# Kernel tuning notes

Measured on AMD Instinct MI355X. Metric: run time of the kernel, lower is better.

The kernel has to match this reference:

```python
import jax, jax.numpy as jnp
import numpy as np

FEATURES = 32
RES = 512
TIME_DIM = 16
N_PTS = 1048576


def _sample_plane(plane, gx, gy):
    """Bilinear grid_sample, align_corners=True.
    plane: (C, H, W); gx in [-1,1] indexes W, gy in [-1,1] indexes H.
    Returns (N, C).
    """
    C, H, W = plane.shape
    ix = (gx + 1.0) * 0.5 * (W - 1)
    iy = (gy + 1.0) * 0.5 * (H - 1)
    ix0f = jnp.clip(jnp.floor(ix), 0, W - 1)
    iy0f = jnp.clip(jnp.floor(iy), 0, H - 1)
    ix0 = ix0f.astype(jnp.int32)
    iy0 = iy0f.astype(jnp.int32)
    ix1 = jnp.minimum(ix0 + 1, W - 1)
    iy1 = jnp.minimum(iy0 + 1, H - 1)
    wx = ix - ix0f  # (N,)
    wy = iy - iy0f
    v00 = plane[:, iy0, ix0]  # (C, N)
    v01 = plane[:, iy0, ix1]
    v10 = plane[:, iy1, ix0]
    v11 = plane[:, iy1, ix1]
    out = (v00 * ((1 - wx) * (1 - wy)) + v01 * (wx * (1 - wy))
           + v10 * ((1 - wx) * wy) + v11 * (wx * wy))
    return out.T  # (N, C)


def setup_inputs() -> dict:
    key = jax.random.key(0)
    ks = jax.random.split(key, 7)
    x = jax.random.uniform(ks[0], (N_PTS, 4), dtype=jnp.float32, minval=-1.0, maxval=1.0)
    plane_xy = jax.random.normal(ks[1], (FEATURES, RES, RES), dtype=jnp.float32)
    plane_xz = jax.random.normal(ks[2], (FEATURES, RES, RES), dtype=jnp.float32)
    plane_yz = jax.random.normal(ks[3], (FEATURES, RES, RES), dtype=jnp.float32)
    plane_xt = jax.random.normal(ks[4], (FEATURES, RES, TIME_DIM), dtype=jnp.float32)
    plane_yt = jax.random.normal(ks[5], (FEATURES, RES, TIME_DIM), dtype=jnp.float32)
    plane_zt = jax.random.normal(ks[6], (FEATURES, RES, TIME_DIM), dtype=jnp.float32)
    return {"x": x, "plane_xy": plane_xy, "plane_xz": plane_xz, "plane_yz": plane_yz,
            "plane_xt": plane_xt, "plane_yt": plane_yt, "plane_zt": plane_zt}


def reference(x, plane_xy, plane_xz, plane_yz, plane_xt, plane_yt, plane_zt):
    center, scale = 0.0, 2.0
    u = (x - center) / scale + 0.5   # map to [0,1]
    g = u * 2.0 - 1.0                # back to [-1,1] grid coords
    gx, gy, gz, gt = g[:, 0], g[:, 1], g[:, 2], g[:, 3]
    feat_xy = _sample_plane(plane_xy, gx, gy)
    feat_xz = _sample_plane(plane_xz, gx, gz)
    feat_yz = _sample_plane(plane_yz, gy, gz)
    feat_xt = _sample_plane(plane_xt, gx, gt)
    feat_yt = _sample_plane(plane_yt, gy, gt)
    feat_zt = _sample_plane(plane_zt, gz, gt)
    return jnp.concatenate([feat_xy, feat_xz, feat_yz, feat_xt, feat_yt, feat_zt], axis=1)
```

## Files before the change

kernel.cpp:

```cpp
#include <hip/hip_runtime.h>
#include <stdint.h>

#define NPTS 1048576

using u16x8 = __attribute__((ext_vector_type(8))) unsigned short;
using f32x4 = __attribute__((ext_vector_type(4))) float;

__device__ __forceinline__ float bf2f(unsigned short u) {
    union { unsigned int i; float f; } c; c.i = ((unsigned int)u) << 16; return c.f;
}
__device__ __forceinline__ unsigned int f2bf_bits(float f) {
    union { float f; unsigned int i; } c; c.f = f;
    unsigned int i = c.i;
    i += 0x7fffu + ((i >> 16) & 1u);
    return i >> 16;
}

template<int WC, int H, int W>
__global__ __launch_bounds__(256) void transpose3(const float* __restrict__ s0,
                                                  const float* __restrict__ s1,
                                                  const float* __restrict__ s2,
                                                  unsigned short* __restrict__ dst) {
    __shared__ float tile[32][WC + 1];
    const float* src = (blockIdx.y == 0) ? s0 : (blockIdx.y == 1) ? s1 : s2;
    constexpr int CH = W / WC;
    const int h  = blockIdx.x / CH;
    const int w0 = (blockIdx.x % CH) * WC;
    const int HW = H * W;
    const float* s = src + h * W + w0;
    for (int i = threadIdx.x; i < 32 * WC; i += 256) {
        int c = i / WC, w = i - c * WC;
        tile[c][w] = s[c * HW + w];
    }
    __syncthreads();
    unsigned int* d = (unsigned int*)(dst + (size_t)blockIdx.y * HW * 32
                                          + (size_t)(h * W + w0) * 32);
    for (int i = threadIdx.x; i < 16 * WC; i += 256) {
        int w = i >> 4, cp = i & 15;
        unsigned int lo = f2bf_bits(tile[cp * 2][w]);
        unsigned int hi = f2bf_bits(tile[cp * 2 + 1][w]);
        d[i] = lo | (hi << 16);
    }
}

template<int W, int H>
__device__ __forceinline__ void sample_one(const unsigned short* __restrict__ pl,
                                           float gw, float gh, int sub,
                                           float* __restrict__ o) {
    float ix = (gw + 1.0f) * 0.5f * (float)(W - 1);
    float iy = (gh + 1.0f) * 0.5f * (float)(H - 1);
    float fx0 = fminf(fmaxf(floorf(ix), 0.0f), (float)(W - 1));
    float fy0 = fminf(fmaxf(floorf(iy), 0.0f), (float)(H - 1));
    int ix0 = (int)fx0, iy0 = (int)fy0;
    int ix1 = min(ix0 + 1, W - 1), iy1 = min(iy0 + 1, H - 1);
    float wx = ix - fx0, wy = iy - fy0;
    float wx0 = 1.0f - wx, wy0 = 1.0f - wy;
    float w00 = wx0 * wy0, w01 = wx * wy0, w10 = wx0 * wy, w11 = wx * wy;
    const int base = sub * 8;
    u16x8 v00 = *(const u16x8*)(pl + ((iy0 * W + ix0) * 32 + base));
    u16x8 v01 = *(const u16x8*)(pl + ((iy0 * W + ix1) * 32 + base));
    u16x8 v10 = *(const u16x8*)(pl + ((iy1 * W + ix0) * 32 + base));
    u16x8 v11 = *(const u16x8*)(pl + ((iy1 * W + ix1) * 32 + base));
    f32x4 r0, r1;
#pragma unroll
    for (int j = 0; j < 4; ++j)
        r0[j] = bf2f(v00[j]) * w00 + bf2f(v01[j]) * w01
              + bf2f(v10[j]) * w10 + bf2f(v11[j]) * w11;
#pragma unroll
    for (int j = 0; j < 4; ++j)
        r1[j] = bf2f(v00[4 + j]) * w00 + bf2f(v01[4 + j]) * w01
              + bf2f(v10[4 + j]) * w10 + bf2f(v11[4 + j]) * w11;
    *(f32x4*)(o)     = r0;
    *(f32x4*)(o + 4) = r1;
}

__global__ __launch_bounds__(256) void sample_kernel(const float* __restrict__ x,
                                                     const unsigned short* __restrict__ ws,
                                                     float* __restrict__ out) {
    int tid = blockIdx.x * 256 + threadIdx.x;
    int p   = tid >> 2;
    int sub = tid & 3;
    f32x4 xv = *(const f32x4*)(x + (size_t)p * 4);
    float gx = (xv[0] * 0.5f + 0.5f) * 2.0f - 1.0f;
    float gy = (xv[1] * 0.5f + 0.5f) * 2.0f - 1.0f;
    float gz = (xv[2] * 0.5f + 0.5f) * 2.0f - 1.0f;
    float gt = (xv[3] * 0.5f + 0.5f) * 2.0f - 1.0f;
    float* o = out + (size_t)p * 192 + sub * 8;
    sample_one<512, 512>(ws + 0ul,        gx, gy, sub, o + 0);
    sample_one<512, 512>(ws + 8388608ul,  gx, gz, sub, o + 32);
    sample_one<512, 512>(ws + 16777216ul, gy, gz, sub, o + 64);
    sample_one<16,  512>(ws + 25165824ul, gx, gt, sub, o + 96);
    sample_one<16,  512>(ws + 25427968ul, gy, gt, sub, o + 128);
    sample_one<16,  512>(ws + 25690112ul, gz, gt, sub, o + 160);
}

template<int W, int H>
__device__ __forceinline__ void sample_direct_one(const float* __restrict__ pl,
                                                  float gw, float gh, int sub,
                                                  float* __restrict__ o) {
    float ix = (gw + 1.0f) * 0.5f * (float)(W - 1);
    float iy = (gh + 1.0f) * 0.5f * (float)(H - 1);
    float fx0 = fminf(fmaxf(floorf(ix), 0.0f), (float)(W - 1));
    float fy0 = fminf(fmaxf(floorf(iy), 0.0f), (float)(H - 1));
    int ix0 = (int)fx0, iy0 = (int)fy0;
    int ix1 = min(ix0 + 1, W - 1), iy1 = min(iy0 + 1, H - 1);
    float wx = ix - fx0, wy = iy - fy0;
    float wx0 = 1.0f - wx, wy0 = 1.0f - wy;
    float w00 = wx0 * wy0, w01 = wx * wy0, w10 = wx0 * wy, w11 = wx * wy;
    const int HW = W * H;
    int a00 = iy0 * W + ix0, a01 = iy0 * W + ix1;
    int a10 = iy1 * W + ix0, a11 = iy1 * W + ix1;
    const float* b = pl + (size_t)sub * 8 * HW;
#pragma unroll
    for (int j = 0; j < 8; ++j) {
        o[j] = b[a00] * w00 + b[a01] * w01 + b[a10] * w10 + b[a11] * w11;
        b += HW;
    }
}

__global__ __launch_bounds__(256) void sample_fallback(const float* __restrict__ x,
    const float* __restrict__ pxy, const float* __restrict__ pxz,
    const float* __restrict__ pyz, const float* __restrict__ pxt,
    const float* __restrict__ pyt, const float* __restrict__ pzt,
    float* __restrict__ out) {
    int tid = blockIdx.x * 256 + threadIdx.x;
    int p   = tid >> 2;
    int sub = tid & 3;
    f32x4 xv = *(const f32x4*)(x + (size_t)p * 4);
    float gx = (xv[0] * 0.5f + 0.5f) * 2.0f - 1.0f;
    float gy = (xv[1] * 0.5f + 0.5f) * 2.0f - 1.0f;
    float gz = (xv[2] * 0.5f + 0.5f) * 2.0f - 1.0f;
    float gt = (xv[3] * 0.5f + 0.5f) * 2.0f - 1.0f;
    float* o = out + (size_t)p * 192 + sub * 8;
    sample_direct_one<512, 512>(pxy, gx, gy, sub, o + 0);
    sample_direct_one<512, 512>(pxz, gx, gz, sub, o + 32);
    sample_direct_one<512, 512>(pyz, gy, gz, sub, o + 64);
    sample_direct_one<16,  512>(pxt, gx, gt, sub, o + 96);
    sample_direct_one<16,  512>(pyt, gy, gt, sub, o + 128);
    sample_direct_one<16,  512>(pzt, gz, gt, sub, o + 160);
}

extern "C" void kernel_launch(void* const* d_in, const int* in_sizes, int n_in,
                              void* d_out, int out_size, void* d_ws, size_t ws_size,
                              hipStream_t stream) {
    const float* x   = (const float*)d_in[0];
    const float* pxy = (const float*)d_in[1];
    const float* pxz = (const float*)d_in[2];
    const float* pyz = (const float*)d_in[3];
    const float* pxt = (const float*)d_in[4];
    const float* pyt = (const float*)d_in[5];
    const float* pzt = (const float*)d_in[6];
    float* out = (float*)d_out;

    const size_t need_elems = 25952256ull;
    const size_t need_bytes = need_elems * 2;

    if (ws_size >= need_bytes) {
        unsigned short* ws = (unsigned short*)d_ws;
        transpose3<64, 512, 512><<<dim3(512 * 8, 3), 256, 0, stream>>>(pxy, pxz, pyz, ws);
        transpose3<16, 512, 16><<<dim3(512, 3), 256, 0, stream>>>(pxt, pyt, pzt, ws + 25165824ul);
        sample_kernel<<<(NPTS * 4) / 256, 256, 0, stream>>>(x, ws, out);
    } else {
        sample_fallback<<<(NPTS * 4) / 256, 256, 0, stream>>>(x, pxy, pxz, pyz, pxt, pyt, pzt, out);
    }
}
```

Measured before the change: 394.0 us.

## Sort points by Morton bin before sampling to improve gather locality

Adds a counting sort of query points into 32^3 Morton-ordered spatial bins (histogram, single-block scan, atomic scatter), then samples in sorted order and writes each result back to its original row. Neighbouring threads then gather nearby plane texels, which is meant to raise cache hit rates for the random bilinear gathers over roughly 50 MB of bf16 planes. Output stores become nontemporal, and workgroups are swizzled across XCDs. The cost is three extra kernels, a memset, atomics, and scattered output writes, and the larger workspace must be available for the new path to run.

```diff
diff --git a/kernel.cpp b/kernel.cpp
--- a/kernel.cpp
+++ b/kernel.cpp
@@ -2,9 +2,18 @@
 #include <stdint.h>
 
 #define NPTS 1048576
+#define NBINS 32768
 
 using u16x8 = __attribute__((ext_vector_type(8))) unsigned short;
 using f32x4 = __attribute__((ext_vector_type(4))) float;
+
+#define OFF_HIST     51904512ul
+#define OFF_CURSOR   52035584ul
+#define OFF_KEYS     52166656ul
+#define OFF_XS       54263808ul
+#define OFF_PID      71041024ul
+#define WS_NEED_FULL 75235328ul
+#define WS_NEED_MID  51904512ul
 
 __device__ __forceinline__ float bf2f(unsigned short u) {
     union { unsigned int i; float f; } c; c.i = ((unsigned int)u) << 16; return c.f;
@@ -14,6 +23,13 @@
     unsigned int i = c.i;
     i += 0x7fffu + ((i >> 16) & 1u);
     return i >> 16;
+}
+__device__ __forceinline__ unsigned int spread3(unsigned int v) {
+    v &= 31u;
+    v = (v | (v << 8)) & 0x100Fu;
+    v = (v | (v << 4)) & 0x10C3u;
+    v = (v | (v << 2)) & 0x1249u;
+    return v;
 }
 
 template<int WC, int H, int W>
@@ -43,7 +59,56 @@
     }
 }
 
-template<int W, int H>
+__global__ __launch_bounds__(256) void hist_kernel(const float* __restrict__ x,
+                                                   unsigned int* __restrict__ hist,
+                                                   unsigned short* __restrict__ keys) {
+    int p = blockIdx.x * 256 + threadIdx.x;
+    f32x4 xv = *(const f32x4*)(x + (size_t)p * 4);
+    int bx = min(31, max(0, (int)((xv[0] + 1.0f) * 16.0f)));
+    int by = min(31, max(0, (int)((xv[1] + 1.0f) * 16.0f)));
+    int bz = min(31, max(0, (int)((xv[2] + 1.0f) * 16.0f)));
+    unsigned int key = (spread3(bx) << 2) | (spread3(by) << 1) | spread3(bz);
+    keys[p] = (unsigned short)key;
+    atomicAdd(&hist[key], 1u);
+}
+
+__global__ __launch_bounds__(1024) void scan_kernel(const unsigned int* __restrict__ hist,
+                                                    unsigned int* __restrict__ cursor) {
+    __shared__ unsigned int part[1024];
+    int t = threadIdx.x;
+    unsigned int local[32];
+    unsigned int s = 0;
+    int base = t * 32;
+#pragma unroll
+    for (int j = 0; j < 32; ++j) { local[j] = s; s += hist[base + j]; }
+    part[t] = s;
+    __syncthreads();
+    for (int off = 1; off < 1024; off <<= 1) {
+        unsigned int v = 0;
+        if (t >= off) v = part[t - off];
+        __syncthreads();
+        if (t >= off) part[t] += v;
+        __syncthreads();
+    }
+    unsigned int chunkbase = part[t] - s;
+#pragma unroll
+    for (int j = 0; j < 32; ++j) cursor[base + j] = chunkbase + local[j];
+}
+
+__global__ __launch_bounds__(256) void scatter_kernel(const float* __restrict__ x,
+                                                      const unsigned short* __restrict__ keys,
+                                                      unsigned int* __restrict__ cursor,
+                                                      f32x4* __restrict__ xs,
+                                                      unsigned int* __restrict__ pid) {
+    int p = blockIdx.x * 256 + threadIdx.x;
+    f32x4 xv = *(const f32x4*)(x + (size_t)p * 4);
+    unsigned int k = keys[p];
+    unsigned int pos = atomicAdd(&cursor[k], 1u);
+    xs[pos] = xv;
+    pid[pos] = (unsigned int)p;
+}
+
+template<int W, int H, bool NT>
 __device__ __forceinline__ void sample_one(const unsigned short* __restrict__ pl,
                                            float gw, float gh, int sub,
                                            float* __restrict__ o) {
@@ -70,8 +135,44 @@
     for (int j = 0; j < 4; ++j)
         r1[j] = bf2f(v00[4 + j]) * w00 + bf2f(v01[4 + j]) * w01
               + bf2f(v10[4 + j]) * w10 + bf2f(v11[4 + j]) * w11;
-    *(f32x4*)(o)     = r0;
-    *(f32x4*)(o + 4) = r1;
+    if (NT) {
+        __builtin_nontemporal_store(r0, (f32x4*)(o));
+        __builtin_nontemporal_store(r1, (f32x4*)(o + 4));
+    } else {
+        *(f32x4*)(o)     = r0;
+        *(f32x4*)(o + 4) = r1;
+    }
+}
+
+__device__ __forceinline__ void sample_all(f32x4 xv, int sub,
+                                           const unsigned short* __restrict__ ws,
+                                           float* __restrict__ o) {
+    float gx = (xv[0] * 0.5f + 0.5f) * 2.0f - 1.0f;
+    float gy = (xv[1] * 0.5f + 0.5f) * 2.0f - 1.0f;
+    float gz = (xv[2] * 0.5f + 0.5f) * 2.0f - 1.0f;
+    float gt = (xv[3] * 0.5f + 0.5f) * 2.0f - 1.0f;
+    sample_one<512, 512, true>(ws + 0ul,        gx, gy, sub, o + 0);
+    sample_one<512, 512, true>(ws + 8388608ul,  gx, gz, sub, o + 32);
+    sample_one<512, 512, true>(ws + 16777216ul, gy, gz, sub, o + 64);
+    sample_one<16,  512, true>(ws + 25165824ul, gx, gt, sub, o + 96);
+    sample_one<16,  512, true>(ws + 25427968ul, gy, gt, sub, o + 128);
+    sample_one<16,  512, true>(ws + 25690112ul, gz, gt, sub, o + 160);
+}
+
+__global__ __launch_bounds__(256) void sample_sorted(const f32x4* __restrict__ xs,
+                                                     const unsigned int* __restrict__ pid,
+                                                     const unsigned short* __restrict__ ws,
+                                                     float* __restrict__ out) {
+    int nwg = gridDim.x;
+    int cpx = nwg >> 3;
+    int bid = blockIdx.x;
+    int swz = (bid & 7) * cpx + (bid >> 3);
+    int tid = swz * 256 + threadIdx.x;
+    int s   = tid >> 2;
+    int sub = tid & 3;
+    f32x4 xv = xs[s];
+    int p = pid[s];
+    sample_all(xv, sub, ws, out + (size_t)p * 192 + sub * 8);
 }
 
 __global__ __launch_bounds__(256) void sample_kernel(const float* __restrict__ x,
@@ -81,17 +182,7 @@
     int p   = tid >> 2;
     int sub = tid & 3;
     f32x4 xv = *(const f32x4*)(x + (size_t)p * 4);
-    float gx = (xv[0] * 0.5f + 0.5f) * 2.0f - 1.0f;
-    float gy = (xv[1] * 0.5f + 0.5f) * 2.0f - 1.0f;
-    float gz = (xv[2] * 0.5f + 0.5f) * 2.0f - 1.0f;
-    float gt = (xv[3] * 0.5f + 0.5f) * 2.0f - 1.0f;
-    float* o = out + (size_t)p * 192 + sub * 8;
-    sample_one<512, 512>(ws + 0ul,        gx, gy, sub, o + 0);
-    sample_one<512, 512>(ws + 8388608ul,  gx, gz, sub, o + 32);
-    sample_one<512, 512>(ws + 16777216ul, gy, gz, sub, o + 64);
-    sample_one<16,  512>(ws + 25165824ul, gx, gt, sub, o + 96);
-    sample_one<16,  512>(ws + 25427968ul, gy, gt, sub, o + 128);
-    sample_one<16,  512>(ws + 25690112ul, gz, gt, sub, o + 160);
+    sample_all(xv, sub, ws, out + (size_t)p * 192 + sub * 8);
 }
 
 template<int W, int H>
@@ -152,14 +243,27 @@
     const float* pzt = (const float*)d_in[6];
     float* out = (float*)d_out;
 
-    const size_t need_elems = 25952256ull;
-    const size_t need_bytes = need_elems * 2;
-
-    if (ws_size >= need_bytes) {
-        unsigned short* ws = (unsigned short*)d_ws;
-        transpose3<64, 512, 512><<<dim3(512 * 8, 3), 256, 0, stream>>>(pxy, pxz, pyz, ws);
-        transpose3<16, 512, 16><<<dim3(512, 3), 256, 0, stream>>>(pxt, pyt, pzt, ws + 25165824ul);
-        sample_kernel<<<(NPTS * 4) / 256, 256, 0, stream>>>(x, ws, out);
+    if (ws_size >= WS_NEED_FULL) {
+        char* wsb = (char*)d_ws;
+        unsigned short* planes = (unsigned short*)wsb;
+        unsigned int*   hist   = (unsigned int*)(wsb + OFF_HIST);
+        unsigned int*   cursor = (unsigned int*)(wsb + OFF_CURSOR);
+        unsigned short* keys   = (unsigned short*)(wsb + OFF_KEYS);
+        f32x4*          xs     = (f32x4*)(wsb + OFF_XS);
+        unsigned int*   pid    = (unsigned int*)(wsb + OFF_PID);
+
+        hipMemsetAsync(hist, 0, NBINS * sizeof(unsigned int), stream);
+        transpose3<64, 512, 512><<<dim3(512 * 8, 3), 256, 0, stream>>>(pxy, pxz, pyz, planes);
+        transpose3<16, 512, 16><<<dim3(512, 3), 256, 0, stream>>>(pxt, pyt, pzt, planes + 25165824ul);
+        hist_kernel<<<NPTS / 256, 256, 0, stream>>>(x, hist, keys);
+        scan_kernel<<<1, 1024, 0, stream>>>(hist, cursor);
+        scatter_kernel<<<NPTS / 256, 256, 0, stream>>>(x, keys, cursor, xs, pid);
+        sample_sorted<<<(NPTS * 4) / 256, 256, 0, stream>>>(xs, pid, planes, out);
+    } else if (ws_size >= WS_NEED_MID) {
+        unsigned short* planes = (unsigned short*)d_ws;
+        transpose3<64, 512, 512><<<dim3(512 * 8, 3), 256, 0, stream>>>(pxy, pxz, pyz, planes);
+        transpose3<16, 512, 16><<<dim3(512, 3), 256, 0, stream>>>(pxt, pyt, pzt, planes + 25165824ul);
+        sample_kernel<<<(NPTS * 4) / 256, 256, 0, stream>>>(x, planes, out);
     } else {
         sample_fallback<<<(NPTS * 4) / 256, 256, 0, stream>>>(x, pxy, pxz, pyz, pxt, pyt, pzt, out);
     }
```

Result: faster. 372.6 us (-5.4%).

## Store horizontally duplicated texel pairs in bf16 workspace to halve gather addresses

Applied to the files above, without the earlier changes.

Adds a transpose pass that writes each texel together with its right neighbour, 64 bf16 channels per entry. Each corner pair (x0,x1) then comes from one contiguous 128-byte span, so the sampler needs two distinct row addresses instead of four scattered ones, which should cut cache-line fetches for the random gathers. In exchange the workspace doubles to about 104 MB and the transpose writes twice as many bytes. Output stores also become nontemporal.

```diff
diff --git a/kernel.cpp b/kernel.cpp
--- a/kernel.cpp
+++ b/kernel.cpp
@@ -5,6 +5,22 @@
 
 using u16x8 = __attribute__((ext_vector_type(8))) unsigned short;
 using f32x4 = __attribute__((ext_vector_type(4))) float;
+
+#define DUP_XY 0ul
+#define DUP_XZ 16777216ul
+#define DUP_YZ 33554432ul
+#define DUP_XT 50331648ul
+#define DUP_YT 50855936ul
+#define DUP_ZT 51380224ul
+#define WS_NEED_FULL 103809024ul
+
+#define PL_XY 0ul
+#define PL_XZ 8388608ul
+#define PL_YZ 16777216ul
+#define PL_XT 25165824ul
+#define PL_YT 25427968ul
+#define PL_ZT 25690112ul
+#define WS_NEED_MID  51904512ul
 
 __device__ __forceinline__ float bf2f(unsigned short u) {
     union { unsigned int i; float f; } c; c.i = ((unsigned int)u) << 16; return c.f;
@@ -14,6 +30,88 @@
     unsigned int i = c.i;
     i += 0x7fffu + ((i >> 16) & 1u);
     return i >> 16;
+}
+
+template<int WC, int W>
+__global__ __launch_bounds__(256) void transpose_dup(const float* __restrict__ s0,
+                                                     const float* __restrict__ s1,
+                                                     const float* __restrict__ s2,
+                                                     unsigned short* __restrict__ dst,
+                                                     size_t planeStride) {
+    __shared__ float tile[32][WC + 2];
+    const float* src = (blockIdx.y == 0) ? s0 : (blockIdx.y == 1) ? s1 : s2;
+    constexpr int CH = W / WC;
+    const int h  = blockIdx.x / CH;
+    const int w0 = (blockIdx.x % CH) * WC;
+    const int HW = 512 * W;
+    for (int i = threadIdx.x; i < 32 * (WC + 1); i += 256) {
+        int c = i / (WC + 1), w = i - c * (WC + 1);
+        int gw = min(w0 + w, W - 1);
+        tile[c][w] = src[c * HW + h * W + gw];
+    }
+    __syncthreads();
+    unsigned int* d = (unsigned int*)(dst + blockIdx.y * planeStride
+                                          + (size_t)(h * W + w0) * 64);
+    for (int idx = threadIdx.x; idx < WC * 32; idx += 256) {
+        int blk = idx >> 5, j = idx & 31;
+        int texsel = j >> 4, chp = j & 15;
+        int col = blk + texsel;
+        unsigned int lo = f2bf_bits(tile[chp * 2][col]);
+        unsigned int hi = f2bf_bits(tile[chp * 2 + 1][col]);
+        d[idx] = lo | (hi << 16);
+    }
+}
+
+template<int W>
+__device__ __forceinline__ void sample_dup(const unsigned short* __restrict__ pl,
+                                           float gw, float gh, int sub,
+                                           float* __restrict__ o) {
+    float ix = (gw + 1.0f) * 0.5f * (float)(W - 1);
+    float iy = (gh + 1.0f) * 0.5f * 511.0f;
+    float fx0 = fminf(fmaxf(floorf(ix), 0.0f), (float)(W - 1));
+    float fy0 = fminf(fmaxf(floorf(iy), 0.0f), 511.0f);
+    int ix0 = (int)fx0, iy0 = (int)fy0;
+    int iy1 = min(iy0 + 1, 511);
+    float wx = ix - fx0, wy = iy - fy0;
+    float wx0 = 1.0f - wx, wy0 = 1.0f - wy;
+    float w00 = wx0 * wy0, w01 = wx * wy0, w10 = wx0 * wy, w11 = wx * wy;
+    const unsigned short* b0 = pl + ((size_t)(iy0 * W + ix0) << 6) + sub * 8;
+    const unsigned short* b1 = pl + ((size_t)(iy1 * W + ix0) << 6) + sub * 8;
+    u16x8 v00 = *(const u16x8*)(b0);
+    u16x8 v01 = *(const u16x8*)(b0 + 32);
+    u16x8 v10 = *(const u16x8*)(b1);
+    u16x8 v11 = *(const u16x8*)(b1 + 32);
+    f32x4 r0, r1;
+#pragma unroll
+    for (int j = 0; j < 4; ++j)
+        r0[j] = bf2f(v00[j]) * w00 + bf2f(v01[j]) * w01
+              + bf2f(v10[j]) * w10 + bf2f(v11[j]) * w11;
+#pragma unroll
+    for (int j = 0; j < 4; ++j)
+        r1[j] = bf2f(v00[4 + j]) * w00 + bf2f(v01[4 + j]) * w01
+              + bf2f(v10[4 + j]) * w10 + bf2f(v11[4 + j]) * w11;
+    __builtin_nontemporal_store(r0, (f32x4*)(o));
+    __builtin_nontemporal_store(r1, (f32x4*)(o + 4));
+}
+
+__global__ __launch_bounds__(256) void sample_dup_kernel(const float* __restrict__ x,
+                                                         const unsigned short* __restrict__ ws,
+                                                         float* __restrict__ out) {
+    int tid = blockIdx.x * 256 + threadIdx.x;
+    int p   = tid >> 2;
+    int sub = tid & 3;
+    f32x4 xv = *(const f32x4*)(x + (size_t)p * 4);
+    float gx = (xv[0] * 0.5f + 0.5f) * 2.0f - 1.0f;
+    float gy = (xv[1] * 0.5f + 0.5f) * 2.0f - 1.0f;
+    float gz = (xv[2] * 0.5f + 0.5f) * 2.0f - 1.0f;
+    float gt = (xv[3] * 0.5f + 0.5f) * 2.0f - 1.0f;
+    float* o = out + (size_t)p * 192 + sub * 8;
+    sample_dup<512>(ws + DUP_XY, gx, gy, sub, o + 0);
+    sample_dup<512>(ws + DUP_XZ, gx, gz, sub, o + 32);
+    sample_dup<512>(ws + DUP_YZ, gy, gz, sub, o + 64);
+    sample_dup<16 >(ws + DUP_XT, gx, gt, sub, o + 96);
+    sample_dup<16 >(ws + DUP_YT, gy, gt, sub, o + 128);
+    sample_dup<16 >(ws + DUP_ZT, gz, gt, sub, o + 160);
 }
 
 template<int WC, int H, int W>
@@ -86,12 +184,12 @@
     float gz = (xv[2] * 0.5f + 0.5f) * 2.0f - 1.0f;
     float gt = (xv[3] * 0.5f + 0.5f) * 2.0f - 1.0f;
     float* o = out + (size_t)p * 192 + sub * 8;
-    sample_one<512, 512>(ws + 0ul,        gx, gy, sub, o + 0);
-    sample_one<512, 512>(ws + 8388608ul,  gx, gz, sub, o + 32);
-    sample_one<512, 512>(ws + 16777216ul, gy, gz, sub, o + 64);
-    sample_one<16,  512>(ws + 25165824ul, gx, gt, sub, o + 96);
-    sample_one<16,  512>(ws + 25427968ul, gy, gt, sub, o + 128);
-    sample_one<16,  512>(ws + 25690112ul, gz, gt, sub, o + 160);
+    sample_one<512, 512>(ws + PL_XY, gx, gy, sub, o + 0);
+    sample_one<512, 512>(ws + PL_XZ, gx, gz, sub, o + 32);
+    sample_one<512, 512>(ws + PL_YZ, gy, gz, sub, o + 64);
+    sample_one<16,  512>(ws + PL_XT, gx, gt, sub, o + 96);
+    sample_one<16,  512>(ws + PL_YT, gy, gt, sub, o + 128);
+    sample_one<16,  512>(ws + PL_ZT, gz, gt, sub, o + 160);
 }
 
 template<int W, int H>
@@ -152,14 +250,18 @@
     const float* pzt = (const float*)d_in[6];
     float* out = (float*)d_out;
 
-    const size_t need_elems = 25952256ull;
-    const size_t need_bytes = need_elems * 2;
-
-    if (ws_size >= need_bytes) {
+    if (ws_size >= WS_NEED_FULL) {
         unsigned short* ws = (unsigned short*)d_ws;
-        transpose3<64, 512, 512><<<dim3(512 * 8, 3), 256, 0, stream>>>(pxy, pxz, pyz, ws);
-        transpose3<16, 512, 16><<<dim3(512, 3), 256, 0, stream>>>(pxt, pyt, pzt, ws + 25165824ul);
-        sample_kernel<<<(NPTS * 4) / 256, 256, 0, stream>>>(x, ws, out);
+        transpose_dup<64, 512><<<dim3(512 * 8, 3), 256, 0, stream>>>(
+            pxy, pxz, pyz, ws + DUP_XY, 16777216ul);
+        transpose_dup<16, 16><<<dim3(512, 3), 256, 0, stream>>>(
+            pxt, pyt, pzt, ws + DUP_XT, 524288ul);
+        sample_dup_kernel<<<(NPTS * 4) / 256, 256, 0, stream>>>(x, ws, out);
+    } else if (ws_size >= WS_NEED_MID) {
+        unsigned short* planes = (unsigned short*)d_ws;
+        transpose3<64, 512, 512><<<dim3(512 * 8, 3), 256, 0, stream>>>(pxy, pxz, pyz, planes);
+        transpose3<16, 512, 16><<<dim3(512, 3), 256, 0, stream>>>(pxt, pyt, pzt, planes + PL_XT);
+        sample_kernel<<<(NPTS * 4) / 256, 256, 0, stream>>>(x, planes, out);
     } else {
         sample_fallback<<<(NPTS * 4) / 256, 256, 0, stream>>>(x, pxy, pxz, pyz, pxt, pyt, pzt, out);
     }
```

New measurement: 351.0 us (median of 2 runs). 1.12x faster.
